# Kernel optimization log

Measured on AMD Instinct MI355X. Metric: run time of the kernel, lower is better.

Reference implementation:

```python
import jax, jax.numpy as jnp
import numpy as np

EPS = 1e-12  # matches torch F.normalize default eps

def setup_inputs() -> dict:
    key = jax.random.key(0)
    k1, k2 = jax.random.split(key)
    query = jax.random.normal(k1, (8, 2048, 512), dtype=jnp.float32)
    support = jax.random.normal(k2, (8, 4096, 512), dtype=jnp.float32)
    return {"query": query, "support": support}

def _l2_normalize(x):
    # torch.nn.functional.normalize(x, dim=-1): x / max(||x||, eps)
    n = jnp.sqrt(jnp.sum(x * x, axis=-1, keepdims=True))
    return x / jnp.maximum(n, EPS)

def reference(query, support):
    # cosine distance: 1 - q_hat @ s_hat^T  -> [B, Nq, Ns]
    qn = _l2_normalize(query)
    sn = _l2_normalize(support)
    dist = 1.0 - jnp.einsum('bqd,bsd->bqs', qn, sn)
    min_d = jnp.min(dist, axis=2)        # [B, Nq]
    return jnp.mean(min_d, axis=1)       # [B]
```

## Files before the change

### kernel.cpp

```cpp
#include <hip/hip_runtime.h>
#include <hip/hip_bf16.h>

typedef __attribute__((ext_vector_type(8))) short short8;
typedef __attribute__((ext_vector_type(4))) float f32x4;
typedef __attribute__((ext_vector_type(16))) float f32x16;
typedef __attribute__((ext_vector_type(8))) int int8v;

#define D   512
#define NQ  2048
#define NS  4096
#define NB  8
#define BM  128
#define BN  128
#define BK  32

typedef const __attribute__((address_space(1))) unsigned int gas_uint;
typedef __attribute__((address_space(3))) unsigned int las_uint;

#define WAIT_VM4   0x0F74
#define WAIT_VM0   0x0F70
#define WAIT_LGKM0 0xC07F

__device__ __forceinline__ short f2bf(float f) {
  unsigned u = __builtin_bit_cast(unsigned, f);
  unsigned r = u + 0x7fffu + ((u >> 16) & 1u);
  return (short)(r >> 16);
}

__device__ __forceinline__ short8 pack8(float4 a, float4 b, float r) {
  short8 o;
  o[0] = f2bf(a.x * r); o[1] = f2bf(a.y * r); o[2] = f2bf(a.z * r); o[3] = f2bf(a.w * r);
  o[4] = f2bf(b.x * r); o[5] = f2bf(b.y * r); o[6] = f2bf(b.z * r); o[7] = f2bf(b.w * r);
  return o;
}

__global__ void normcvt8_kernel(const float* __restrict__ q, const float* __restrict__ s,
                                unsigned char* __restrict__ qn, unsigned char* __restrict__ sn,
                                unsigned* __restrict__ maxenc) {
  if (blockIdx.x < 64) maxenc[(blockIdx.x << 8) | threadIdx.x] = 0;
  int wave = blockIdx.x * 4 + (threadIdx.x >> 6);
  int lane = threadIdx.x & 63;
  const int NQR = NB * NQ;
  const float4* src; unsigned char* dst;
  if (wave < NQR) { src = (const float4*)(q + (size_t)wave * D); dst = qn + (size_t)wave * D; }
  else {
    size_t w = wave - NQR;
    src = (const float4*)(s + w * D); dst = sn + w * D;
  }
  float4 a = src[lane * 2];
  float4 b = src[lane * 2 + 1];
  float ss = a.x*a.x + a.y*a.y + a.z*a.z + a.w*a.w
           + b.x*b.x + b.y*b.y + b.z*b.z + b.w*b.w;
  #pragma unroll
  for (int m = 32; m >= 1; m >>= 1) ss += __shfl_xor(ss, m, 64);
  float r = 1.0f / fmaxf(sqrtf(ss), 1e-12f);
  int w0 = __builtin_amdgcn_cvt_pk_fp8_f32(a.x * r, a.y * r, 0, false);
  w0     = __builtin_amdgcn_cvt_pk_fp8_f32(a.z * r, a.w * r, w0, true);
  int w1 = __builtin_amdgcn_cvt_pk_fp8_f32(b.x * r, b.y * r, 0, false);
  w1     = __builtin_amdgcn_cvt_pk_fp8_f32(b.z * r, b.w * r, w1, true);
  *(int2*)(dst + lane * 8) = make_int2(w0, w1);
}

__global__ __launch_bounds__(256) void cosmax7_kernel(
    const unsigned char* __restrict__ Qn, const unsigned char* __restrict__ Sn,
    unsigned int* __restrict__ maxenc)
{
  __shared__ __align__(16) unsigned char sbuf[49152];
  __shared__ float maxbuf[64][2];

  const int b   = blockIdx.z;
  const int mt  = blockIdx.y;
  const int nsp = blockIdx.x;
  const int tid  = threadIdx.x;
  const int wave = tid >> 6;
  const int lane = tid & 63;
  const int l31 = lane & 31, kc = lane >> 5;
  const int mstrip = wave & 1, nhalf = wave >> 1;

  {
    const unsigned char* Qbase = Qn + ((size_t)b * NQ + (size_t)mt * 64) * D;
    const int baserow = wave * 2 + (lane >> 5);
    #pragma unroll
    for (int p = 0; p < 8; ++p) {
      int row = p * 8 + baserow;
      int g   = (lane & 31) ^ (row & 31);
      __builtin_amdgcn_global_load_lds(
          (gas_uint*)(Qbase + (size_t)row * D + g * 16),
          (las_uint*)(sbuf + 16384 + p * 4096 + wave * 1024), 16, 0, 0);
    }
  }
  __syncthreads();

  const int srow8 = lane >> 3;
  const int sch   = (lane & 7) ^ srow8;
  const unsigned char* gS = Sn +
      ((size_t)b * NS + (size_t)nsp * 2048 + wave * 32 + srow8) * D + sch * 16;

  auto issue = [&](size_t goff, int ldsoff) {
    #pragma unroll
    for (int t = 0; t < 4; ++t)
      __builtin_amdgcn_global_load_lds((gas_uint*)(gS + goff + (size_t)t * 4096),
          (las_uint*)(sbuf + ldsoff + wave * 4096 + t * 1024), 16, 0, 0);
  };

  issue(0, 0);

  const int arow = mstrip * 32 + l31;
  int8v a[8];
  #pragma unroll
  for (int kk = 0; kk < 8; ++kk) {
    int c0 = (4 * kk + 2 * kc) ^ l31;
    ((int4*)&a[kk])[0] = *(const int4*)&sbuf[16384 + arow * 512 + c0 * 16];
    ((int4*)&a[kk])[1] = *(const int4*)&sbuf[16384 + arow * 512 + (c0 ^ 1) * 16];
  }
  __builtin_amdgcn_s_waitcnt(WAIT_LGKM0);
  asm volatile("" ::: "memory");
  __builtin_amdgcn_s_barrier();
  asm volatile("" ::: "memory");
  issue(128, 16384);

  const int brow0 = (nhalf * 64 + l31) * 128;
  const int brow1 = brow0 + 4096;
  const int cxor  = ((kc * 2) ^ (l31 & 7)) * 16;

  f32x16 acc0, acc1;
  float rmax[16];
  #pragma unroll
  for (int r = 0; r < 16; ++r) rmax[r] = -2.0f;

  int rd = 0, wr = 32768;

  auto computeK = [&](int kt, int rdo) {
    const unsigned char* Bb = sbuf + rdo;
    #pragma unroll
    for (int ss = 0; ss < 2; ++ss) {
      const int cb = cxor ^ (ss * 64);
      int8v b0, b1;
      ((int4*)&b0)[0] = *(const int4*)&Bb[brow0 + cb];
      ((int4*)&b0)[1] = *(const int4*)&Bb[brow0 + (cb ^ 16)];
      ((int4*)&b1)[0] = *(const int4*)&Bb[brow1 + cb];
      ((int4*)&b1)[1] = *(const int4*)&Bb[brow1 + (cb ^ 16)];
      acc0 = __builtin_amdgcn_mfma_scale_f32_32x32x64_f8f6f4(
          a[kt * 2 + ss], b0, acc0, 0, 0, 0, 0x7f7f7f7f, 0, 0x7f7f7f7f);
      acc1 = __builtin_amdgcn_mfma_scale_f32_32x32x64_f8f6f4(
          a[kt * 2 + ss], b1, acc1, 0, 0, 0, 0x7f7f7f7f, 0, 0x7f7f7f7f);
    }
  };

  #define ROT(x) x = (x == 32768) ? 0 : x + 16384

  for (int nt2 = 0; nt2 < 16; ++nt2) {
    const size_t ntb = (size_t)nt2 << 16;

    __builtin_amdgcn_s_waitcnt(WAIT_VM4);
    asm volatile("" ::: "memory");
    __builtin_amdgcn_s_barrier();
    asm volatile("" ::: "memory");
    issue(ntb + 256, wr); ROT(wr);
    #pragma unroll
    for (int r = 0; r < 16; ++r) { acc0[r] = 0.f; acc1[r] = 0.f; }
    computeK(0, rd); ROT(rd);

    __builtin_amdgcn_s_waitcnt(WAIT_VM4);
    asm volatile("" ::: "memory");
    __builtin_amdgcn_s_barrier();
    asm volatile("" ::: "memory");
    issue(ntb + 384, wr); ROT(wr);
    computeK(1, rd); ROT(rd);

    __builtin_amdgcn_s_waitcnt(WAIT_VM4);
    asm volatile("" ::: "memory");
    __builtin_amdgcn_s_barrier();
    asm volatile("" ::: "memory");
    if (nt2 < 15) { issue(ntb + 65536, wr); ROT(wr); }
    computeK(2, rd); ROT(rd);

    if (nt2 < 15) __builtin_amdgcn_s_waitcnt(WAIT_VM4);
    else          __builtin_amdgcn_s_waitcnt(WAIT_VM0);
    asm volatile("" ::: "memory");
    __builtin_amdgcn_s_barrier();
    asm volatile("" ::: "memory");
    if (nt2 < 15) { issue(ntb + 65536 + 128, wr); ROT(wr); }
    computeK(3, rd); ROT(rd);

    #pragma unroll
    for (int r = 0; r < 16; ++r)
      rmax[r] = fmaxf(rmax[r], fmaxf(acc0[r], acc1[r]));
  }
  #undef ROT

  #pragma unroll
  for (int r = 0; r < 16; ++r) {
    float v = rmax[r];
    v = fmaxf(v, __shfl_xor(v, 1, 64));
    v = fmaxf(v, __shfl_xor(v, 2, 64));
    v = fmaxf(v, __shfl_xor(v, 4, 64));
    v = fmaxf(v, __shfl_xor(v, 8, 64));
    v = fmaxf(v, __shfl_xor(v, 16, 64));
    if (l31 == 0)
      maxbuf[mstrip * 32 + (r & 3) + 8 * (r >> 2) + 4 * kc][nhalf] = v;
  }
  __syncthreads();

  if (tid < 64) {
    float v = fmaxf(maxbuf[tid][0], maxbuf[tid][1]);
    unsigned e = __builtin_bit_cast(unsigned, v);
    e = ((int)e >= 0) ? (e | 0x80000000u) : ~e;
    atomicMax(&maxenc[(size_t)b * NQ + (size_t)mt * 64 + tid], e);
  }
}

__global__ void finalize_kernel(const unsigned* __restrict__ maxenc,
                                float* __restrict__ out) {
  int b = blockIdx.x;
  int tid = threadIdx.x;
  float sum = 0.f;
  for (int i = tid; i < NQ; i += 256) {
    unsigned e = maxenc[(size_t)b * NQ + i];
    unsigned u = (e & 0x80000000u) ? (e & 0x7fffffffu) : ~e;
    float v = __builtin_bit_cast(float, u);
    sum += 1.0f - v;
  }
  #pragma unroll
  for (int m = 32; m >= 1; m >>= 1) sum += __shfl_xor(sum, m, 64);
  __shared__ float part[4];
  if ((tid & 63) == 0) part[tid >> 6] = sum;
  __syncthreads();
  if (tid == 0) out[b] = (part[0] + part[1] + part[2] + part[3]) * (1.0f / (float)NQ);
}

__global__ void norms_kernel(const float* __restrict__ q, const float* __restrict__ s,
                             float* __restrict__ rq, float* __restrict__ rs) {
  int wave = blockIdx.x * 4 + (threadIdx.x >> 6);
  int lane = threadIdx.x & 63;
  const int NQR = NB * NQ, NSR = NB * NS;
  if (wave >= NQR + NSR) return;
  const float4* r4; float* outp;
  if (wave < NQR) { r4 = (const float4*)(q + (size_t)wave * D); outp = rq + wave; }
  else           { r4 = (const float4*)(s + (size_t)(wave - NQR) * D); outp = rs + (wave - NQR); }
  float4 a = r4[lane];
  float4 b = r4[lane + 64];
  float ss = a.x*a.x + a.y*a.y + a.z*a.z + a.w*a.w
           + b.x*b.x + b.y*b.y + b.z*b.z + b.w*b.w;
  #pragma unroll
  for (int m = 32; m >= 1; m >>= 1) ss += __shfl_xor(ss, m, 64);
  if (lane == 0) *outp = 1.0f / fmaxf(sqrtf(ss), 1e-12f);
}

__global__ __launch_bounds__(256, 3) void cosmax_kernel(
    const float* __restrict__ Q, const float* __restrict__ S,
    const float* __restrict__ rq, const float* __restrict__ rs,
    unsigned int* __restrict__ maxenc)
{
  __shared__ short As[BM * BK];
  __shared__ short Bs[BN * BK];
  __shared__ float maxbuf[BM][2];

  const int b  = blockIdx.z, mt = blockIdx.y, nt = blockIdx.x;
  const float* Qb  = Q + ((size_t)b * NQ + mt * BM) * D;
  const float* Sb  = S + ((size_t)b * NS + nt * BN) * D;
  const float* rqb = rq + (size_t)b * NQ + mt * BM;
  const float* rsb = rs + (size_t)b * NS + nt * BN;

  const int tid  = threadIdx.x;
  const int srow = tid >> 2;
  const int kseg = (tid & 3) * 8;
  const float rq0 = rqb[srow], rq1 = rqb[srow + 64];
  const float rs0 = rsb[srow], rs1 = rsb[srow + 64];
  const int wave = tid >> 6, lane = tid & 63;
  const int wm = (wave & 1) * 64, wn = (wave >> 1) * 64;
  const int lm = lane & 15, lk = (lane >> 4) * 8;

  f32x4 acc[4][4];
  #pragma unroll
  for (int i = 0; i < 4; ++i)
    #pragma unroll
    for (int j = 0; j < 4; ++j) acc[i][j] = (f32x4){0.f, 0.f, 0.f, 0.f};

  const float* qrow0 = Qb + (size_t)srow * D + kseg;
  const float* qrow1 = qrow0 + (size_t)64 * D;
  const float* srow0 = Sb + (size_t)srow * D + kseg;
  const float* srow1 = srow0 + (size_t)64 * D;

  float4 qa, qb2, qc, qd, sa, sb2, sc, sd;
  #define LOADK(k0)                                                    \
    qa  = *(const float4*)(qrow0 + (k0));  qb2 = *(const float4*)(qrow0 + (k0) + 4); \
    qc  = *(const float4*)(qrow1 + (k0));  qd  = *(const float4*)(qrow1 + (k0) + 4); \
    sa  = *(const float4*)(srow0 + (k0));  sb2 = *(const float4*)(srow0 + (k0) + 4); \
    sc  = *(const float4*)(srow1 + (k0));  sd  = *(const float4*)(srow1 + (k0) + 4);
  LOADK(0);
  #pragma unroll 4
  for (int kt = 0; kt < D / BK; ++kt) {
    *(short8*)&As[srow        * BK + kseg] = pack8(qa, qb2, rq0);
    *(short8*)&As[(srow + 64) * BK + kseg] = pack8(qc, qd,  rq1);
    *(short8*)&Bs[srow        * BK + kseg] = pack8(sa, sb2, rs0);
    *(short8*)&Bs[(srow + 64) * BK + kseg] = pack8(sc, sd,  rs1);
    __syncthreads();
    if (kt < D / BK - 1) { LOADK((kt + 1) * BK); }
    short8 af[4], bf[4];
    #pragma unroll
    for (int i = 0; i < 4; ++i) af[i] = *(short8*)&As[(wm + i * 16 + lm) * BK + lk];
    #pragma unroll
    for (int j = 0; j < 4; ++j) bf[j] = *(short8*)&Bs[(wn + j * 16 + lm) * BK + lk];
    #pragma unroll
    for (int i = 0; i < 4; ++i)
      #pragma unroll
      for (int j = 0; j < 4; ++j)
        acc[i][j] = __builtin_amdgcn_mfma_f32_16x16x32_bf16(af[i], bf[j], acc[i][j], 0, 0, 0);
    __syncthreads();
  }
  #undef LOADK

  #pragma unroll
  for (int i = 0; i < 4; ++i) {
    #pragma unroll
    for (int r = 0; r < 4; ++r) {
      float v = fmaxf(fmaxf(acc[i][0][r], acc[i][1][r]),
                      fmaxf(acc[i][2][r], acc[i][3][r]));
      v = fmaxf(v, __shfl_xor(v, 1, 64));
      v = fmaxf(v, __shfl_xor(v, 2, 64));
      v = fmaxf(v, __shfl_xor(v, 4, 64));
      v = fmaxf(v, __shfl_xor(v, 8, 64));
      if ((lane & 15) == 0) {
        int row = wm + i * 16 + (lane >> 4) * 4 + r;
        maxbuf[row][wave >> 1] = v;
      }
    }
  }
  __syncthreads();
  if (tid < BM) {
    float v = fmaxf(maxbuf[tid][0], maxbuf[tid][1]);
    unsigned e = __builtin_bit_cast(unsigned, v);
    e = ((int)e >= 0) ? (e | 0x80000000u) : ~e;
    atomicMax(&maxenc[(size_t)b * NQ + mt * BM + tid], e);
  }
}

extern "C" void kernel_launch(void* const* d_in, const int* in_sizes, int n_in,
                              void* d_out, int out_size, void* d_ws, size_t ws_size,
                              hipStream_t stream) {
  const float* q = (const float*)d_in[0];
  const float* s = (const float*)d_in[1];
  float* out = (float*)d_out;

  unsigned* maxenc = (unsigned*)d_ws;
  const size_t QOFF = 65536;
  const size_t SOFF = QOFF + (size_t)NB * NQ * D;
  const size_t NEED = SOFF + (size_t)NB * NS * D;

  if (ws_size >= NEED) {
    unsigned char* qn = (unsigned char*)d_ws + QOFF;
    unsigned char* sn = (unsigned char*)d_ws + SOFF;
    normcvt8_kernel<<<NB * (NQ + NS) / 4, 256, 0, stream>>>(q, s, qn, sn, maxenc);
    dim3 grid7(2, NQ / 64, NB);
    cosmax7_kernel<<<grid7, 256, 0, stream>>>(qn, sn, maxenc);
    finalize_kernel<<<NB, 256, 0, stream>>>(maxenc, out);
  } else {
    float* rq = (float*)((char*)d_ws + 65536);
    float* rs = (float*)((char*)d_ws + 131072);
    hipMemsetAsync(maxenc, 0, (size_t)NB * NQ * sizeof(unsigned), stream);
    norms_kernel<<<NB * (NQ + NS) / 4, 256, 0, stream>>>(q, s, rq, rs);
    dim3 grid(NS / BN, NQ / BM, NB);
    cosmax_kernel<<<grid, 256, 0, stream>>>(q, s, rq, rs, maxenc);
    finalize_kernel<<<NB, 256, 0, stream>>>(maxenc, out);
  }
}
```

Measured before the change: 166.7 us.

## Deepen LDS pipeline to four stages and remap blocks to batch-fastest order

Grows shared memory to 64KB so four B-tile stages are in flight instead of three, using fixed per-stage offsets in place of rotating pointers. Waits relax to vmcnt 8 so more global-to-LDS loads overlap with MFMA work. The grid becomes 1D with batch as the fastest index, which changes which blocks run together and how they share L2. The larger LDS footprint may lower occupancy, and loop unrolling is disabled.

```diff
diff --git a/kernel.cpp b/kernel.cpp
--- a/kernel.cpp
+++ b/kernel.cpp
@@ -17,6 +17,7 @@
 typedef const __attribute__((address_space(1))) unsigned int gas_uint;
 typedef __attribute__((address_space(3))) unsigned int las_uint;
 
+#define WAIT_VM8   0x0F78
 #define WAIT_VM4   0x0F74
 #define WAIT_VM0   0x0F70
 #define WAIT_LGKM0 0xC07F
@@ -61,16 +62,18 @@
   *(int2*)(dst + lane * 8) = make_int2(w0, w1);
 }
 
-__global__ __launch_bounds__(256) void cosmax7_kernel(
+__global__ __launch_bounds__(256) void cosmax11_kernel(
     const unsigned char* __restrict__ Qn, const unsigned char* __restrict__ Sn,
     unsigned int* __restrict__ maxenc)
 {
-  __shared__ __align__(16) unsigned char sbuf[49152];
+  __shared__ __align__(16) unsigned char sbuf[65536];
   __shared__ float maxbuf[64][2];
 
-  const int b   = blockIdx.z;
-  const int mt  = blockIdx.y;
-  const int nsp = blockIdx.x;
+  const int id  = blockIdx.x;
+  const int b   = id & 7;
+  const int j   = id >> 3;
+  const int mt  = j & 31;
+  const int nsp = j >> 5;
   const int tid  = threadIdx.x;
   const int wave = tid >> 6;
   const int lane = tid & 63;
@@ -118,6 +121,7 @@
   __builtin_amdgcn_s_barrier();
   asm volatile("" ::: "memory");
   issue(128, 16384);
+  issue(256, 32768);
 
   const int brow0 = (nhalf * 64 + l31) * 128;
   const int brow1 = brow0 + 4096;
@@ -127,8 +131,6 @@
   float rmax[16];
   #pragma unroll
   for (int r = 0; r < 16; ++r) rmax[r] = -2.0f;
-
-  int rd = 0, wr = 32768;
 
   auto computeK = [&](int kt, int rdo) {
     const unsigned char* Bb = sbuf + rdo;
@@ -147,47 +149,47 @@
     }
   };
 
-  #define ROT(x) x = (x == 32768) ? 0 : x + 16384
-
+  #pragma clang loop unroll(disable)
   for (int nt2 = 0; nt2 < 16; ++nt2) {
     const size_t ntb = (size_t)nt2 << 16;
-
-    __builtin_amdgcn_s_waitcnt(WAIT_VM4);
+    const bool more = (nt2 < 15);
+
+    __builtin_amdgcn_s_waitcnt(WAIT_VM8);
     asm volatile("" ::: "memory");
     __builtin_amdgcn_s_barrier();
     asm volatile("" ::: "memory");
-    issue(ntb + 256, wr); ROT(wr);
+    issue(ntb + 384, 49152);
     #pragma unroll
     for (int r = 0; r < 16; ++r) { acc0[r] = 0.f; acc1[r] = 0.f; }
-    computeK(0, rd); ROT(rd);
-
-    __builtin_amdgcn_s_waitcnt(WAIT_VM4);
+    computeK(0, 0);
+
+    __builtin_amdgcn_s_waitcnt(WAIT_VM8);
     asm volatile("" ::: "memory");
     __builtin_amdgcn_s_barrier();
     asm volatile("" ::: "memory");
-    issue(ntb + 384, wr); ROT(wr);
-    computeK(1, rd); ROT(rd);
-
-    __builtin_amdgcn_s_waitcnt(WAIT_VM4);
+    if (more) issue(ntb + 65536, 0);
+    computeK(1, 16384);
+
+    if (more) __builtin_amdgcn_s_waitcnt(WAIT_VM8);
+    else      __builtin_amdgcn_s_waitcnt(WAIT_VM4);
     asm volatile("" ::: "memory");
     __builtin_amdgcn_s_barrier();
     asm volatile("" ::: "memory");
-    if (nt2 < 15) { issue(ntb + 65536, wr); ROT(wr); }
-    computeK(2, rd); ROT(rd);
-
-    if (nt2 < 15) __builtin_amdgcn_s_waitcnt(WAIT_VM4);
-    else          __builtin_amdgcn_s_waitcnt(WAIT_VM0);
+    if (more) issue(ntb + 65536 + 128, 16384);
+    computeK(2, 32768);
+
+    if (more) __builtin_amdgcn_s_waitcnt(WAIT_VM8);
+    else      __builtin_amdgcn_s_waitcnt(WAIT_VM0);
     asm volatile("" ::: "memory");
     __builtin_amdgcn_s_barrier();
     asm volatile("" ::: "memory");
-    if (nt2 < 15) { issue(ntb + 65536 + 128, wr); ROT(wr); }
-    computeK(3, rd); ROT(rd);
+    if (more) issue(ntb + 65536 + 256, 32768);
+    computeK(3, 49152);
 
     #pragma unroll
     for (int r = 0; r < 16; ++r)
       rmax[r] = fmaxf(rmax[r], fmaxf(acc0[r], acc1[r]));
   }
-  #undef ROT
 
   #pragma unroll
   for (int r = 0; r < 16; ++r) {
@@ -352,8 +354,7 @@
     unsigned char* qn = (unsigned char*)d_ws + QOFF;
     unsigned char* sn = (unsigned char*)d_ws + SOFF;
     normcvt8_kernel<<<NB * (NQ + NS) / 4, 256, 0, stream>>>(q, s, qn, sn, maxenc);
-    dim3 grid7(2, NQ / 64, NB);
-    cosmax7_kernel<<<grid7, 256, 0, stream>>>(qn, sn, maxenc);
+    cosmax11_kernel<<<512, 256, 0, stream>>>(qn, sn, maxenc);
     finalize_kernel<<<NB, 256, 0, stream>>>(maxenc, out);
   } else {
     float* rq = (float*)((char*)d_ws + 65536);
```

Result: faster. 161.1 us (-3.4%).
